# Kernel tuning notes

Hardware: AMD Instinct MI355X
Metric: run time of the kernel (lower is better)

## Reference

```python
import jax, jax.numpy as jnp
import numpy as np
from jax import lax

B, C_IN, C_OUT, H, W, K, PAD = 4, 64, 64, 96, 96, 3, 1
K2 = K * K


def setup_inputs() -> dict:
    key = jax.random.key(0)
    k1, k2, k3, k4, k5 = jax.random.split(key, 5)
    x = jax.random.normal(k1, (B, C_IN, H, W), jnp.float32)
    offset = jax.random.normal(k2, (B, 2 * K2, H, W), jnp.float32)
    weight = jax.random.normal(k3, (C_OUT, C_IN, K, K), jnp.float32) * 0.05
    mask_weight = jax.random.normal(k4, (K2, C_IN, K, K), jnp.float32) * 0.05
    mask_bias = jax.random.normal(k5, (K2,), jnp.float32) * 0.05
    return {"x": x, "offset": offset, "weight": weight,
            "mask_weight": mask_weight, "mask_bias": mask_bias}


def _deform_conv2d(x, offset, weight, mask):
    # torchvision ordering: per kernel tap k, offset[:, 2k] is dy, offset[:, 2k+1] is dx
    off_y = offset[:, 0::2]  # [B, K2, H, W]
    off_x = offset[:, 1::2]
    ky, kx = jnp.meshgrid(jnp.arange(K), jnp.arange(K), indexing="ij")
    ky = ky.reshape(K2).astype(x.dtype)
    kx = kx.reshape(K2).astype(x.dtype)
    hh = jnp.arange(H, dtype=x.dtype)
    ww = jnp.arange(W, dtype=x.dtype)
    base_y = hh[None, :, None] - PAD + ky[:, None, None]   # [K2, H, 1]
    base_x = ww[None, None, :] - PAD + kx[:, None, None]   # [K2, 1, W]
    py = base_y[None] + off_y                               # [B, K2, H, W]
    px = base_x[None] + off_x

    y0 = jnp.floor(py)
    x0 = jnp.floor(px)
    wy = py - y0   # bilinear weights
    wx = px - x0
    y0i = y0.astype(jnp.int32)
    x0i = x0.astype(jnp.int32)

    x_flat = x.reshape(B, C_IN, H * W)

    def gather(yy, xx):
        valid = (yy >= 0) & (yy < H) & (xx >= 0) & (xx < W)
        idx = jnp.clip(yy, 0, H - 1) * W + jnp.clip(xx, 0, W - 1)  # [B,K2,H,W]
        idx_f = idx.reshape(B, -1)
        v = jax.vmap(lambda xf, i: xf[:, i])(x_flat, idx_f)  # [B, C, K2*H*W]
        v = v.reshape(B, C_IN, K2, H, W)
        return v * valid[:, None].astype(v.dtype)

    v00 = gather(y0i, x0i)
    v01 = gather(y0i, x0i + 1)
    v10 = gather(y0i + 1, x0i)
    v11 = gather(y0i + 1, x0i + 1)

    wy_ = wy[:, None]  # [B,1,K2,H,W]
    wx_ = wx[:, None]
    sampled = (v00 * (1 - wy_) * (1 - wx_) + v01 * (1 - wy_) * wx_
               + v10 * wy_ * (1 - wx_) + v11 * wy_ * wx_)
    sampled = sampled * mask[:, None]  # modulate by sigmoid mask

    w2 = weight.reshape(C_OUT, C_IN, K2)
    return jnp.einsum("bckhw,ock->bohw", sampled, w2)


def reference(x, offset, weight, mask_weight, mask_bias):
    mask_logits = lax.conv_general_dilated(
        x, mask_weight, window_strides=(1, 1), padding=[(PAD, PAD), (PAD, PAD)],
        dimension_numbers=("NCHW", "OIHW", "NCHW"))
    mask = jax.nn.sigmoid(mask_logits + mask_bias[None, :, None, None])
    return _deform_conv2d(x, offset, weight, mask)
```

## Files before the change

kernel.cpp:

```cpp
#include <hip/hip_runtime.h>
#include <math.h>

#define BB 4
#define CI 64
#define CO 64
#define HH 96
#define WW 96
#define HW (HH*WW)
#define K2 9
#define TPX 16
#define NTT (HW/TPX)
#define NTP 288
#define PADC 1

typedef __attribute__((ext_vector_type(8))) short short8;
typedef __attribute__((ext_vector_type(4))) float float4v;

#define XT_USHORTS ((size_t)BB*HW*64)
#define WF_USHORTS (18*64*32)
#define MWF_USHORTS (18*16*32)

__device__ __forceinline__ float bf2f(short s) {
    return __uint_as_float(((unsigned int)(unsigned short)s) << 16);
}
__device__ __forceinline__ short f2bf(float f) {
    unsigned int u = __float_as_uint(f);
    u = (u + 0x7fffu + ((u >> 16) & 1u)) >> 16;
    return (short)u;
}

__device__ __forceinline__ void unswz16(int bid, int* b, int* tile) {
    int g = bid & 7, r = bid >> 3;
    *b = g & 3;
    *tile = (g >> 2) * 288 + r;
}
__device__ __forceinline__ void unswz32(int bid, int* b, int* tile) {
    int g = bid & 7, r = bid >> 3;
    *b = g & 3;
    *tile = (g >> 2) * 144 + r;
}

#define PBASE (BB*NTP)
__global__ __launch_bounds__(256) void prep_kernel(const float* __restrict__ x,
                                                   const float* __restrict__ wgt,
                                                   const float* __restrict__ mw,
                                                   unsigned short* __restrict__ xT,
                                                   unsigned short* __restrict__ Wf,
                                                   unsigned short* __restrict__ MWf) {
    __shared__ unsigned short ts[32][72];
    int t = threadIdx.x;
    if (blockIdx.x < PBASE) {
        int b, tl; unswz32(blockIdx.x, &b, &tl);
        int p0 = tl * 32;
        const float* xb = x + (size_t)b * CI * HW + p0;
        int c0 = t >> 3, pq = t & 7;
        #pragma unroll
        for (int i = 0; i < 2; i++) {
            int c = c0 + i * 32;
            float4v v = *(const float4v*)(xb + (size_t)c * HW + pq * 4);
            ts[pq * 4 + 0][c] = (unsigned short)f2bf(v[0]);
            ts[pq * 4 + 1][c] = (unsigned short)f2bf(v[1]);
            ts[pq * 4 + 2][c] = (unsigned short)f2bf(v[2]);
            ts[pq * 4 + 3][c] = (unsigned short)f2bf(v[3]);
        }
        __syncthreads();
        int px = t >> 3, cq = t & 7;
        unsigned short* xo = xT + ((size_t)b * HW + p0 + px) * 64 + cq * 8;
        *(short8*)xo = *(const short8*)&ts[px][cq * 8];
    } else {
        int i = (blockIdx.x - PBASE) * 256 + t;
        if (i < WF_USHORTS) {
            int frag = i >> 11;
            int o = (i >> 5) & 63;
            int tt = i & 31;
            int k = frag >> 1, cc = frag & 1;
            int c = cc * 32 + tt;
            Wf[i] = (unsigned short)f2bf(wgt[o * 576 + c * 9 + k]);
        } else if (i < WF_USHORTS + MWF_USHORTS) {
            int e = i - WF_USHORTS;
            int frag = e >> 9;
            int m = (e >> 5) & 15;
            int tt = e & 31;
            int q = frag >> 1, cc = frag & 1;
            int c = cc * 32 + tt;
            MWf[e] = (m < 9) ? (unsigned short)f2bf(mw[m * 576 + c * 9 + q]) : 0;
        }
    }
}

__global__ __launch_bounds__(256, 6) void fused_kernel(const float* __restrict__ off,
                                                       const float* __restrict__ mbias,
                                                       const unsigned short* __restrict__ xT,
                                                       const unsigned short* __restrict__ Wf,
                                                       const unsigned short* __restrict__ MWf,
                                                       float* __restrict__ out) {
    __shared__ float s_mred[2][2][K2][TPX];
    __shared__ int   s_idx[K2][4][TPX];
    __shared__ float s_w[K2][4][TPX];
    __shared__ float s_part[3][16][64];

    int t = threadIdx.x;
    int lane = t & 63, wv = t >> 6;
    int ch = wv & 1, tg = wv >> 1;
    int n = lane & 15, quad = lane >> 4;
    int b, tl; unswz16(blockIdx.x, &b, &tl);
    int p0 = tl * TPX;
    int p = p0 + n;
    int h = p / WW, wc = p % WW;
    const unsigned short* xTb = xT + (size_t)b * HW * 64;
    int cbase = ch * 32 + quad * 8;

    {
        float4v macc = {0.f, 0.f, 0.f, 0.f};
#define PHASE_A(QB, QE)                                                          \
        _Pragma("unroll")                                                        \
        for (int q = QB; q < QE; q++) {                                          \
            int hh = h + q / 3 - 1, ww2 = wc + q % 3 - 1;                        \
            bool valid = (hh >= 0) && (hh < HH) && (ww2 >= 0) && (ww2 < WW);     \
            int nidx = valid ? (hh * WW + ww2) : 0;                              \
            short8 bfrag = {0, 0, 0, 0, 0, 0, 0, 0};                             \
            if (valid) bfrag = *(const short8*)(xTb + (size_t)nidx * 64 + cbase);\
            short8 afrag = *(const short8*)(MWf +                                \
                ((size_t)((q * 2 + ch) * 16 + n)) * 32 + quad * 8);              \
            macc = __builtin_amdgcn_mfma_f32_16x16x32_bf16(afrag, bfrag, macc, 0, 0, 0); \
        }
        if (tg == 0) { PHASE_A(0, 5) } else { PHASE_A(5, 9) }
        #pragma unroll
        for (int r = 0; r < 4; r++) {
            int row = quad * 4 + r;
            if (row < 9) s_mred[ch][tg][row][n] = macc[r];
        }
    }
    __syncthreads();

    if (t < K2 * TPX) {
        int k = t >> 4, pe = t & 15;
        int pp = p0 + pe;
        int hh0 = pp / WW, ww0 = pp % WW;
        int ky = k / 3, kx = k % 3;
        float oy = off[((size_t)b * 2 * K2 + 2 * k) * HW + pp];
        float ox = off[((size_t)b * 2 * K2 + 2 * k + 1) * HW + pp];
        float s = s_mred[0][0][k][pe] + s_mred[0][1][k][pe] +
                  s_mred[1][0][k][pe] + s_mred[1][1][k][pe] + mbias[k];
        float m = 1.f / (1.f + expf(-s));
        float py = (float)(hh0 - PADC + ky) + oy;
        float pxf = (float)(ww0 - PADC + kx) + ox;
        float y0f = floorf(py), x0f = floorf(pxf);
        float wy = py - y0f, wx = pxf - x0f;
        int y0 = (int)y0f, x0 = (int)x0f;
        int y1 = y0 + 1, x1 = x0 + 1;
        int y0c = min(max(y0, 0), HH - 1), y1c = min(max(y1, 0), HH - 1);
        int x0c = min(max(x0, 0), WW - 1), x1c = min(max(x1, 0), WW - 1);
        bool vy0 = (y0 >= 0) && (y0 < HH), vy1 = (y1 >= 0) && (y1 < HH);
        bool vx0 = (x0 >= 0) && (x0 < WW), vx1 = (x1 >= 0) && (x1 < WW);
        float w00 = (1.f - wy) * (1.f - wx) * m; if (!(vy0 && vx0)) w00 = 0.f;
        float w01 = (1.f - wy) * wx * m;         if (!(vy0 && vx1)) w01 = 0.f;
        float w10 = wy * (1.f - wx) * m;         if (!(vy1 && vx0)) w10 = 0.f;
        float w11 = wy * wx * m;                 if (!(vy1 && vx1)) w11 = 0.f;
        s_idx[k][0][pe] = y0c * WW + x0c;
        s_idx[k][1][pe] = y0c * WW + x1c;
        s_idx[k][2][pe] = y1c * WW + x0c;
        s_idx[k][3][pe] = y1c * WW + x1c;
        s_w[k][0][pe] = w00; s_w[k][1][pe] = w01;
        s_w[k][2][pe] = w10; s_w[k][3][pe] = w11;
    }
    __syncthreads();

    float4v acc0 = {0.f, 0.f, 0.f, 0.f};
    float4v acc1 = {0.f, 0.f, 0.f, 0.f};
    float4v acc2 = {0.f, 0.f, 0.f, 0.f};
    float4v acc3 = {0.f, 0.f, 0.f, 0.f};
    const unsigned short* xq = xTb + cbase;

#define PHASE_C(KB, KE)                                                          \
    _Pragma("unroll")                                                            \
    for (int k = KB; k < KE; k++) {                                              \
        int i0 = s_idx[k][0][n], i1 = s_idx[k][1][n];                            \
        int i2 = s_idx[k][2][n], i3 = s_idx[k][3][n];                            \
        float w0 = s_w[k][0][n], w1 = s_w[k][1][n];                              \
        float w2 = s_w[k][2][n], w3 = s_w[k][3][n];                              \
        short8 u0 = *(const short8*)(xq + (size_t)i0 * 64);                      \
        short8 u1 = *(const short8*)(xq + (size_t)i1 * 64);                      \
        short8 u2 = *(const short8*)(xq + (size_t)i2 * 64);                      \
        short8 u3 = *(const short8*)(xq + (size_t)i3 * 64);                      \
        short8 bfrag;                                                            \
        _Pragma("unroll")                                                        \
        for (int j = 0; j < 8; j++) {                                            \
            float v = bf2f(u0[j]) * w0 + bf2f(u1[j]) * w1 +                      \
                      bf2f(u2[j]) * w2 + bf2f(u3[j]) * w3;                       \
            bfrag[j] = f2bf(v);                                                  \
        }                                                                        \
        const unsigned short* wp = Wf + (size_t)((k * 2 + ch) * 64) * 32 + quad * 8; \
        short8 a0 = *(const short8*)(wp + (0 * 16 + n) * 32);                    \
        short8 a1 = *(const short8*)(wp + (1 * 16 + n) * 32);                    \
        short8 a2 = *(const short8*)(wp + (2 * 16 + n) * 32);                    \
        short8 a3 = *(const short8*)(wp + (3 * 16 + n) * 32);                    \
        acc0 = __builtin_amdgcn_mfma_f32_16x16x32_bf16(a0, bfrag, acc0, 0, 0, 0);\
        acc1 = __builtin_amdgcn_mfma_f32_16x16x32_bf16(a1, bfrag, acc1, 0, 0, 0);\
        acc2 = __builtin_amdgcn_mfma_f32_16x16x32_bf16(a2, bfrag, acc2, 0, 0, 0);\
        acc3 = __builtin_amdgcn_mfma_f32_16x16x32_bf16(a3, bfrag, acc3, 0, 0, 0);\
    }
    if (tg == 0) { PHASE_C(0, 5) } else { PHASE_C(5, 9) }

    if (wv != 0) {
        #pragma unroll
        for (int r = 0; r < 4; r++) {
            s_part[wv - 1][0 * 4 + r][lane] = acc0[r];
            s_part[wv - 1][1 * 4 + r][lane] = acc1[r];
            s_part[wv - 1][2 * 4 + r][lane] = acc2[r];
            s_part[wv - 1][3 * 4 + r][lane] = acc3[r];
        }
    }
    __syncthreads();
    if (wv == 0) {
        float* ob = out + (size_t)b * CO * HW + p0 + n;
        #pragma unroll
        for (int r = 0; r < 4; r++) {
            int j0 = 0 * 4 + r, j1 = 1 * 4 + r, j2 = 2 * 4 + r, j3 = 3 * 4 + r;
            ob[(size_t)(0 * 16 + quad * 4 + r) * HW] =
                acc0[r] + s_part[0][j0][lane] + s_part[1][j0][lane] + s_part[2][j0][lane];
            ob[(size_t)(1 * 16 + quad * 4 + r) * HW] =
                acc1[r] + s_part[0][j1][lane] + s_part[1][j1][lane] + s_part[2][j1][lane];
            ob[(size_t)(2 * 16 + quad * 4 + r) * HW] =
                acc2[r] + s_part[0][j2][lane] + s_part[1][j2][lane] + s_part[2][j2][lane];
            ob[(size_t)(3 * 16 + quad * 4 + r) * HW] =
                acc3[r] + s_part[0][j3][lane] + s_part[1][j3][lane] + s_part[2][j3][lane];
        }
    }
}

extern "C" void kernel_launch(void* const* d_in, const int* in_sizes, int n_in,
                              void* d_out, int out_size, void* d_ws, size_t ws_size,
                              hipStream_t stream) {
    const float* x   = (const float*)d_in[0];
    const float* off = (const float*)d_in[1];
    const float* wgt = (const float*)d_in[2];
    const float* mw  = (const float*)d_in[3];
    const float* mb  = (const float*)d_in[4];
    float* out = (float*)d_out;

    unsigned short* xT  = (unsigned short*)d_ws;
    unsigned short* Wf  = xT + XT_USHORTS;
    unsigned short* MWf = Wf + WF_USHORTS;

    int prep_grid = PBASE + (WF_USHORTS + MWF_USHORTS + 255) / 256;
    hipLaunchKernelGGL(prep_kernel, dim3(prep_grid), dim3(256), 0, stream,
                       x, wgt, mw, xT, Wf, MWf);
    hipLaunchKernelGGL(fused_kernel, dim3(BB * NTT), dim3(256), 0, stream,
                       off, mb, xT, Wf, MWf, out);
}
```

Before: 106.8 us.

## Make fused deform-conv kernel persistent with register-resident weight fragments

The fused kernel becomes a persistent grid of 512 blocks that loop over all pixel tiles. Each wave loads its weight and mask-weight MFMA A-fragments into registers once and reuses them across tiles, instead of reloading them per tile. The aim is to remove repeated weight loads and per-block launch overhead. In exchange, launch bounds drop to 2 blocks per CU, so fewer waves are available to hide gather latency, and 2304 tiles over 512 blocks leaves uneven work per block.

```diff
diff --git a/kernel.cpp b/kernel.cpp
--- a/kernel.cpp
+++ b/kernel.cpp
@@ -10,6 +10,8 @@
 #define K2 9
 #define TPX 16
 #define NTT (HW/TPX)
+#define NTILES (BB*NTT)
+#define GRID 512
 #define NTP 288
 #define PADC 1
 
@@ -29,8 +31,8 @@
     return (short)u;
 }
 
-__device__ __forceinline__ void unswz16(int bid, int* b, int* tile) {
-    int g = bid & 7, r = bid >> 3;
+__device__ __forceinline__ void unswz16(int tt, int* b, int* tile) {
+    int g = tt & 7, r = tt >> 3;
     *b = g & 3;
     *tile = (g >> 2) * 288 + r;
 }
@@ -88,145 +90,171 @@
     }
 }
 
-__global__ __launch_bounds__(256, 6) void fused_kernel(const float* __restrict__ off,
+struct SmemT {
+    float mred[2][2][K2][TPX];
+    int   idx[K2][4][TPX];
+    float w[K2][4][TPX];
+    float part[3][16][64];
+};
+
+template<int KB, int KE>
+__device__ __forceinline__ void tile_work(SmemT& sm, int t, int wv, int ch,
+                                          int tg, int n, int quad,
+                                          const float* __restrict__ off,
+                                          const float* __restrict__ mbias,
+                                          const unsigned short* __restrict__ xT,
+                                          const unsigned short* __restrict__ Wf,
+                                          const unsigned short* __restrict__ MWf,
+                                          float* __restrict__ out, int bid) {
+    constexpr int NK = KE - KB;
+    int lane = t & 63;
+
+    short8 wA[NK][4];
+    short8 mA[NK];
+    #pragma unroll
+    for (int kk = 0; kk < NK; kk++) {
+        int k = KB + kk;
+        const unsigned short* wp = Wf + (size_t)((k * 2 + ch) * 64) * 32 + quad * 8;
+        #pragma unroll
+        for (int s = 0; s < 4; s++)
+            wA[kk][s] = *(const short8*)(wp + (s * 16 + n) * 32);
+        mA[kk] = *(const short8*)(MWf + ((size_t)((k * 2 + ch) * 16 + n)) * 32 + quad * 8);
+    }
+
+    for (int tt = bid; tt < NTILES; tt += GRID) {
+        int b, tl; unswz16(tt, &b, &tl);
+        int p0 = tl * TPX;
+        int p = p0 + n;
+        int h = p / WW, wc = p % WW;
+        const unsigned short* xTb = xT + (size_t)b * HW * 64;
+        int cbase = ch * 32 + quad * 8;
+
+        {
+            float4v macc = {0.f, 0.f, 0.f, 0.f};
+            #pragma unroll
+            for (int kk = 0; kk < NK; kk++) {
+                int q = KB + kk;
+                int hh = h + q / 3 - 1, ww2 = wc + q % 3 - 1;
+                bool valid = (hh >= 0) && (hh < HH) && (ww2 >= 0) && (ww2 < WW);
+                int nidx = valid ? (hh * WW + ww2) : 0;
+                short8 bfrag = {0, 0, 0, 0, 0, 0, 0, 0};
+                if (valid) bfrag = *(const short8*)(xTb + (size_t)nidx * 64 + cbase);
+                macc = __builtin_amdgcn_mfma_f32_16x16x32_bf16(mA[kk], bfrag, macc, 0, 0, 0);
+            }
+            #pragma unroll
+            for (int r = 0; r < 4; r++) {
+                int row = quad * 4 + r;
+                if (row < 9) sm.mred[ch][tg][row][n] = macc[r];
+            }
+        }
+        __syncthreads();
+
+        if (t < K2 * TPX) {
+            int k = t >> 4, pe = t & 15;
+            int pp = p0 + pe;
+            int hh0 = pp / WW, ww0 = pp % WW;
+            int ky = k / 3, kx = k % 3;
+            float oy = off[((size_t)b * 2 * K2 + 2 * k) * HW + pp];
+            float ox = off[((size_t)b * 2 * K2 + 2 * k + 1) * HW + pp];
+            float s = sm.mred[0][0][k][pe] + sm.mred[0][1][k][pe] +
+                      sm.mred[1][0][k][pe] + sm.mred[1][1][k][pe] + mbias[k];
+            float m = 1.f / (1.f + expf(-s));
+            float py = (float)(hh0 - PADC + ky) + oy;
+            float pxf = (float)(ww0 - PADC + kx) + ox;
+            float y0f = floorf(py), x0f = floorf(pxf);
+            float wy = py - y0f, wx = pxf - x0f;
+            int y0 = (int)y0f, x0 = (int)x0f;
+            int y1 = y0 + 1, x1 = x0 + 1;
+            int y0c = min(max(y0, 0), HH - 1), y1c = min(max(y1, 0), HH - 1);
+            int x0c = min(max(x0, 0), WW - 1), x1c = min(max(x1, 0), WW - 1);
+            bool vy0 = (y0 >= 0) && (y0 < HH), vy1 = (y1 >= 0) && (y1 < HH);
+            bool vx0 = (x0 >= 0) && (x0 < WW), vx1 = (x1 >= 0) && (x1 < WW);
+            float w00 = (1.f - wy) * (1.f - wx) * m; if (!(vy0 && vx0)) w00 = 0.f;
+            float w01 = (1.f - wy) * wx * m;         if (!(vy0 && vx1)) w01 = 0.f;
+            float w10 = wy * (1.f - wx) * m;         if (!(vy1 && vx0)) w10 = 0.f;
+            float w11 = wy * wx * m;                 if (!(vy1 && vx1)) w11 = 0.f;
+            sm.idx[k][0][pe] = y0c * WW + x0c;
+            sm.idx[k][1][pe] = y0c * WW + x1c;
+            sm.idx[k][2][pe] = y1c * WW + x0c;
+            sm.idx[k][3][pe] = y1c * WW + x1c;
+            sm.w[k][0][pe] = w00; sm.w[k][1][pe] = w01;
+            sm.w[k][2][pe] = w10; sm.w[k][3][pe] = w11;
+        }
+        __syncthreads();
+
+        float4v acc0 = {0.f, 0.f, 0.f, 0.f};
+        float4v acc1 = {0.f, 0.f, 0.f, 0.f};
+        float4v acc2 = {0.f, 0.f, 0.f, 0.f};
+        float4v acc3 = {0.f, 0.f, 0.f, 0.f};
+        const unsigned short* xq = xTb + cbase;
+
+        #pragma unroll
+        for (int kk = 0; kk < NK; kk++) {
+            int k = KB + kk;
+            int i0 = sm.idx[k][0][n], i1 = sm.idx[k][1][n];
+            int i2 = sm.idx[k][2][n], i3 = sm.idx[k][3][n];
+            float w0 = sm.w[k][0][n], w1 = sm.w[k][1][n];
+            float w2 = sm.w[k][2][n], w3 = sm.w[k][3][n];
+            short8 u0 = *(const short8*)(xq + (size_t)i0 * 64);
+            short8 u1 = *(const short8*)(xq + (size_t)i1 * 64);
+            short8 u2 = *(const short8*)(xq + (size_t)i2 * 64);
+            short8 u3 = *(const short8*)(xq + (size_t)i3 * 64);
+            short8 bfrag;
+            #pragma unroll
+            for (int j = 0; j < 8; j++) {
+                float v = bf2f(u0[j]) * w0 + bf2f(u1[j]) * w1 +
+                          bf2f(u2[j]) * w2 + bf2f(u3[j]) * w3;
+                bfrag[j] = f2bf(v);
+            }
+            acc0 = __builtin_amdgcn_mfma_f32_16x16x32_bf16(wA[kk][0], bfrag, acc0, 0, 0, 0);
+            acc1 = __builtin_amdgcn_mfma_f32_16x16x32_bf16(wA[kk][1], bfrag, acc1, 0, 0, 0);
+            acc2 = __builtin_amdgcn_mfma_f32_16x16x32_bf16(wA[kk][2], bfrag, acc2, 0, 0, 0);
+            acc3 = __builtin_amdgcn_mfma_f32_16x16x32_bf16(wA[kk][3], bfrag, acc3, 0, 0, 0);
+        }
+
+        if (wv != 0) {
+            #pragma unroll
+            for (int r = 0; r < 4; r++) {
+                sm.part[wv - 1][0 * 4 + r][lane] = acc0[r];
+                sm.part[wv - 1][1 * 4 + r][lane] = acc1[r];
+                sm.part[wv - 1][2 * 4 + r][lane] = acc2[r];
+                sm.part[wv - 1][3 * 4 + r][lane] = acc3[r];
+            }
+        }
+        __syncthreads();
+        if (wv == 0) {
+            float* ob = out + (size_t)b * CO * HW + p0 + n;
+            #pragma unroll
+            for (int r = 0; r < 4; r++) {
+                int j0 = r, j1 = 4 + r, j2 = 8 + r, j3 = 12 + r;
+                ob[(size_t)(0 * 16 + quad * 4 + r) * HW] =
+                    acc0[r] + sm.part[0][j0][lane] + sm.part[1][j0][lane] + sm.part[2][j0][lane];
+                ob[(size_t)(1 * 16 + quad * 4 + r) * HW] =
+                    acc1[r] + sm.part[0][j1][lane] + sm.part[1][j1][lane] + sm.part[2][j1][lane];
+                ob[(size_t)(2 * 16 + quad * 4 + r) * HW] =
+                    acc2[r] + sm.part[0][j2][lane] + sm.part[1][j2][lane] + sm.part[2][j2][lane];
+                ob[(size_t)(3 * 16 + quad * 4 + r) * HW] =
+                    acc3[r] + sm.part[0][j3][lane] + sm.part[1][j3][lane] + sm.part[2][j3][lane];
+            }
+        }
+    }
+}
+
+__global__ __launch_bounds__(256, 2) void fused_kernel(const float* __restrict__ off,
                                                        const float* __restrict__ mbias,
                                                        const unsigned short* __restrict__ xT,
                                                        const unsigned short* __restrict__ Wf,
                                                        const unsigned short* __restrict__ MWf,
                                                        float* __restrict__ out) {
-    __shared__ float s_mred[2][2][K2][TPX];
-    __shared__ int   s_idx[K2][4][TPX];
-    __shared__ float s_w[K2][4][TPX];
-    __shared__ float s_part[3][16][64];
-
+    __shared__ SmemT sm;
     int t = threadIdx.x;
     int lane = t & 63, wv = t >> 6;
     int ch = wv & 1, tg = wv >> 1;
     int n = lane & 15, quad = lane >> 4;
-    int b, tl; unswz16(blockIdx.x, &b, &tl);
-    int p0 = tl * TPX;
-    int p = p0 + n;
-    int h = p / WW, wc = p % WW;
-    const unsigned short* xTb = xT + (size_t)b * HW * 64;
-    int cbase = ch * 32 + quad * 8;
-
-    {
-        float4v macc = {0.f, 0.f, 0.f, 0.f};
-#define PHASE_A(QB, QE)                                                          \
-        _Pragma("unroll")                                                        \
-        for (int q = QB; q < QE; q++) {                                          \
-            int hh = h + q / 3 - 1, ww2 = wc + q % 3 - 1;                        \
-            bool valid = (hh >= 0) && (hh < HH) && (ww2 >= 0) && (ww2 < WW);     \
-            int nidx = valid ? (hh * WW + ww2) : 0;                              \
-            short8 bfrag = {0, 0, 0, 0, 0, 0, 0, 0};                             \
-            if (valid) bfrag = *(const short8*)(xTb + (size_t)nidx * 64 + cbase);\
-            short8 afrag = *(const short8*)(MWf +                                \
-                ((size_t)((q * 2 + ch) * 16 + n)) * 32 + quad * 8);              \
-            macc = __builtin_amdgcn_mfma_f32_16x16x32_bf16(afrag, bfrag, macc, 0, 0, 0); \
-        }
-        if (tg == 0) { PHASE_A(0, 5) } else { PHASE_A(5, 9) }
-        #pragma unroll
-        for (int r = 0; r < 4; r++) {
-            int row = quad * 4 + r;
-            if (row < 9) s_mred[ch][tg][row][n] = macc[r];
-        }
-    }
-    __syncthreads();
-
-    if (t < K2 * TPX) {
-        int k = t >> 4, pe = t & 15;
-        int pp = p0 + pe;
-        int hh0 = pp / WW, ww0 = pp % WW;
-        int ky = k / 3, kx = k % 3;
-        float oy = off[((size_t)b * 2 * K2 + 2 * k) * HW + pp];
-        float ox = off[((size_t)b * 2 * K2 + 2 * k + 1) * HW + pp];
-        float s = s_mred[0][0][k][pe] + s_mred[0][1][k][pe] +
-                  s_mred[1][0][k][pe] + s_mred[1][1][k][pe] + mbias[k];
-        float m = 1.f / (1.f + expf(-s));
-        float py = (float)(hh0 - PADC + ky) + oy;
-        float pxf = (float)(ww0 - PADC + kx) + ox;
-        float y0f = floorf(py), x0f = floorf(pxf);
-        float wy = py - y0f, wx = pxf - x0f;
-        int y0 = (int)y0f, x0 = (int)x0f;
-        int y1 = y0 + 1, x1 = x0 + 1;
-        int y0c = min(max(y0, 0), HH - 1), y1c = min(max(y1, 0), HH - 1);
-        int x0c = min(max(x0, 0), WW - 1), x1c = min(max(x1, 0), WW - 1);
-        bool vy0 = (y0 >= 0) && (y0 < HH), vy1 = (y1 >= 0) && (y1 < HH);
-        bool vx0 = (x0 >= 0) && (x0 < WW), vx1 = (x1 >= 0) && (x1 < WW);
-        float w00 = (1.f - wy) * (1.f - wx) * m; if (!(vy0 && vx0)) w00 = 0.f;
-        float w01 = (1.f - wy) * wx * m;         if (!(vy0 && vx1)) w01 = 0.f;
-        float w10 = wy * (1.f - wx) * m;         if (!(vy1 && vx0)) w10 = 0.f;
-        float w11 = wy * wx * m;                 if (!(vy1 && vx1)) w11 = 0.f;
-        s_idx[k][0][pe] = y0c * WW + x0c;
-        s_idx[k][1][pe] = y0c * WW + x1c;
-        s_idx[k][2][pe] = y1c * WW + x0c;
-        s_idx[k][3][pe] = y1c * WW + x1c;
-        s_w[k][0][pe] = w00; s_w[k][1][pe] = w01;
-        s_w[k][2][pe] = w10; s_w[k][3][pe] = w11;
-    }
-    __syncthreads();
-
-    float4v acc0 = {0.f, 0.f, 0.f, 0.f};
-    float4v acc1 = {0.f, 0.f, 0.f, 0.f};
-    float4v acc2 = {0.f, 0.f, 0.f, 0.f};
-    float4v acc3 = {0.f, 0.f, 0.f, 0.f};
-    const unsigned short* xq = xTb + cbase;
-
-#define PHASE_C(KB, KE)                                                          \
-    _Pragma("unroll")                                                            \
-    for (int k = KB; k < KE; k++) {                                              \
-        int i0 = s_idx[k][0][n], i1 = s_idx[k][1][n];                            \
-        int i2 = s_idx[k][2][n], i3 = s_idx[k][3][n];                            \
-        float w0 = s_w[k][0][n], w1 = s_w[k][1][n];                              \
-        float w2 = s_w[k][2][n], w3 = s_w[k][3][n];                              \
-        short8 u0 = *(const short8*)(xq + (size_t)i0 * 64);                      \
-        short8 u1 = *(const short8*)(xq + (size_t)i1 * 64);                      \
-        short8 u2 = *(const short8*)(xq + (size_t)i2 * 64);                      \
-        short8 u3 = *(const short8*)(xq + (size_t)i3 * 64);                      \
-        short8 bfrag;                                                            \
-        _Pragma("unroll")                                                        \
-        for (int j = 0; j < 8; j++) {                                            \
-            float v = bf2f(u0[j]) * w0 + bf2f(u1[j]) * w1 +                      \
-                      bf2f(u2[j]) * w2 + bf2f(u3[j]) * w3;                       \
-            bfrag[j] = f2bf(v);                                                  \
-        }                                                                        \
-        const unsigned short* wp = Wf + (size_t)((k * 2 + ch) * 64) * 32 + quad * 8; \
-        short8 a0 = *(const short8*)(wp + (0 * 16 + n) * 32);                    \
-        short8 a1 = *(const short8*)(wp + (1 * 16 + n) * 32);                    \
-        short8 a2 = *(const short8*)(wp + (2 * 16 + n) * 32);                    \
-        short8 a3 = *(const short8*)(wp + (3 * 16 + n) * 32);                    \
-        acc0 = __builtin_amdgcn_mfma_f32_16x16x32_bf16(a0, bfrag, acc0, 0, 0, 0);\
-        acc1 = __builtin_amdgcn_mfma_f32_16x16x32_bf16(a1, bfrag, acc1, 0, 0, 0);\
-        acc2 = __builtin_amdgcn_mfma_f32_16x16x32_bf16(a2, bfrag, acc2, 0, 0, 0);\
-        acc3 = __builtin_amdgcn_mfma_f32_16x16x32_bf16(a3, bfrag, acc3, 0, 0, 0);\
-    }
-    if (tg == 0) { PHASE_C(0, 5) } else { PHASE_C(5, 9) }
-
-    if (wv != 0) {
-        #pragma unroll
-        for (int r = 0; r < 4; r++) {
-            s_part[wv - 1][0 * 4 + r][lane] = acc0[r];
-            s_part[wv - 1][1 * 4 + r][lane] = acc1[r];
-            s_part[wv - 1][2 * 4 + r][lane] = acc2[r];
-            s_part[wv - 1][3 * 4 + r][lane] = acc3[r];
-        }
-    }
-    __syncthreads();
-    if (wv == 0) {
-        float* ob = out + (size_t)b * CO * HW + p0 + n;
-        #pragma unroll
-        for (int r = 0; r < 4; r++) {
-            int j0 = 0 * 4 + r, j1 = 1 * 4 + r, j2 = 2 * 4 + r, j3 = 3 * 4 + r;
-            ob[(size_t)(0 * 16 + quad * 4 + r) * HW] =
-                acc0[r] + s_part[0][j0][lane] + s_part[1][j0][lane] + s_part[2][j0][lane];
-            ob[(size_t)(1 * 16 + quad * 4 + r) * HW] =
-                acc1[r] + s_part[0][j1][lane] + s_part[1][j1][lane] + s_part[2][j1][lane];
-            ob[(size_t)(2 * 16 + quad * 4 + r) * HW] =
-                acc2[r] + s_part[0][j2][lane] + s_part[1][j2][lane] + s_part[2][j2][lane];
-            ob[(size_t)(3 * 16 + quad * 4 + r) * HW] =
-                acc3[r] + s_part[0][j3][lane] + s_part[1][j3][lane] + s_part[2][j3][lane];
-        }
-    }
+    if (tg == 0)
+        tile_work<0, 5>(sm, t, wv, ch, tg, n, quad, off, mbias, xT, Wf, MWf, out, blockIdx.x);
+    else
+        tile_work<5, 9>(sm, t, wv, ch, tg, n, quad, off, mbias, xT, Wf, MWf, out, blockIdx.x);
 }
 
 extern "C" void kernel_launch(void* const* d_in, const int* in_sizes, int n_in,
@@ -246,6 +274,6 @@
     int prep_grid = PBASE + (WF_USHORTS + MWF_USHORTS + 255) / 256;
     hipLaunchKernelGGL(prep_kernel, dim3(prep_grid), dim3(256), 0, stream,
                        x, wgt, mw, xT, Wf, MWf);
-    hipLaunchKernelGGL(fused_kernel, dim3(BB * NTT), dim3(256), 0, stream,
+    hipLaunchKernelGGL(fused_kernel, dim3(GRID), dim3(256), 0, stream,
                        off, mb, xT, Wf, MWf, out);
 }
```

Result: faster. 103.5 us (-3.0%).
